# Performance work log

Hardware: AMD Instinct MI355X
Metric: run time of the kernel (lower is better)

## Reference

```python
import jax, jax.numpy as jnp
import numpy as np

D = 768       # GATv2 in/out feats (num_heads=1)
D_OUT = 384   # fc output
K = 51        # round(top_rate * L) = round(0.1 * 512)
EPS = 1e-5    # nn.LayerNorm default eps


def _layer_norm(x, g, b):
    mu = jnp.mean(x, axis=-1, keepdims=True)
    var = jnp.mean((x - mu) ** 2, axis=-1, keepdims=True)
    return (x - mu) / jnp.sqrt(var + EPS) * g + b


def setup_inputs() -> dict:
    key = jax.random.key(0)
    ks = jax.random.split(key, 12)
    B, L = 4, 512
    s = 0.02
    return {
        "hidden_state": jax.random.normal(ks[0], (B, L, D), jnp.float32),
        "attention": jax.random.uniform(ks[1], (B, L, L), jnp.float32),
        # GATv2Conv params (fc_src, fc_dst, attn vector, output bias)
        "W_src": jax.random.normal(ks[2], (D, D), jnp.float32) * s,
        "b_src": jnp.zeros((D,), jnp.float32),
        "W_dst": jax.random.normal(ks[3], (D, D), jnp.float32) * s,
        "b_dst": jnp.zeros((D,), jnp.float32),
        "attn_vec": jax.random.normal(ks[4], (D,), jnp.float32) * s,
        "gat_bias": jnp.zeros((D,), jnp.float32),
        # GlobalAttentionPooling gate_nn: Linear(768, 1)
        "gate_W": jax.random.normal(ks[5], (D, 1), jnp.float32) * s,
        "gate_b": jnp.zeros((1,), jnp.float32),
        # LayerNorm(768)
        "ln_g": jnp.ones((D,), jnp.float32),
        "ln_b": jnp.zeros((D,), jnp.float32),
        # fc: Linear(768, 384)
        "fc_W": jax.random.normal(ks[6], (D, D_OUT), jnp.float32) * s,
        "fc_b": jnp.zeros((D_OUT,), jnp.float32),
        # LayerNorm(384)
        "ln2_g": jnp.ones((D_OUT,), jnp.float32),
        "ln2_b": jnp.zeros((D_OUT,), jnp.float32),
        "mask": jnp.ones((B, L), jnp.int32),  # unused by the original forward
        "type": 0,                              # unused string/type flag
    }


def reference(hidden_state, attention, W_src, b_src, W_dst, b_dst, attn_vec,
              gat_bias, gate_W, gate_b, ln_g, ln_b, fc_W, fc_b, ln2_g, ln2_b,
              mask, type):
    B, L, _ = hidden_state.shape
    # --- topk sparsification: each node i keeps K source neighbors ---
    vals, idx = jax.lax.top_k(attention, K)          # [B, L, K]
    valid = vals > 0.0                                # edges kept by pos_sign filter

    # --- GATv2Conv (num_heads=1, residual=Identity since 768==768) ---
    feat_src = hidden_state @ W_src + b_src           # [B, L, D]
    feat_dst = hidden_state @ W_dst + b_dst           # [B, L, D]
    g = feat_src[jnp.arange(B)[:, None, None], idx]   # [B, L, K, D] gathered src feats
    e = jax.nn.leaky_relu(g + feat_dst[:, :, None, :], 0.2)
    scores = jnp.einsum("blkd,d->blk", e, attn_vec)   # [B, L, K]
    scores = jnp.where(valid, scores, -1e9)           # removed edges masked out
    a = jax.nn.softmax(scores, axis=-1)               # edge_softmax per dst node
    h = jnp.einsum("blk,blkd->bld", a, g)             # weighted scatter-sum
    h = h + hidden_state + gat_bias                   # residual (identity) + bias
    h = jax.nn.leaky_relu(h, 0.01)                    # nn.LeakyReLU activation

    # --- GlobalAttentionPooling: softmax(gate) weighted segment reduce ---
    gate = h @ gate_W + gate_b                        # [B, L, 1]
    p = jax.nn.softmax(gate, axis=1)
    pooled = jnp.sum(p * h, axis=1)                   # [B, D]

    # --- head: fc(dropout(ln(relu(out)))) then ln2 (dropout = eval identity) ---
    out = _layer_norm(jax.nn.relu(pooled), ln_g, ln_b)
    out = out @ fc_W + fc_b
    out = _layer_norm(out, ln2_g, ln2_b)
    return out
```

## Files before the change

### kernel.cpp

```cpp
#include <hip/hip_runtime.h>
#include <math.h>

#define D 768
#define DOUT 384
#define LSEQ 512
#define BATCH 4
#define KTOP 51
#define EPS 1e-5f

typedef unsigned short ushort_t;
typedef __bf16 bf16x8 __attribute__((ext_vector_type(8)));
typedef float f32x4 __attribute__((ext_vector_type(4)));

#define GLOAD16(gp, lp)                                                        \
    __builtin_amdgcn_global_load_lds(                                          \
        (const __attribute__((address_space(1))) unsigned int*)(gp),           \
        (__attribute__((address_space(3))) unsigned int*)(lp), 16, 0, 0)

__device__ __forceinline__ ushort_t f2bf(float f) {
    unsigned int u = __builtin_bit_cast(unsigned int, f);
    u = (u + 0x7FFFu + ((u >> 16) & 1u)) >> 16;
    return (ushort_t)u;
}

__device__ __forceinline__ float bf2f(ushort_t u) {
    unsigned int v = ((unsigned int)u) << 16;
    return __builtin_bit_cast(float, v);
}

__global__ __launch_bounds__(256) void prep_kernel(const float* __restrict__ hidden,
                                                   ushort_t* __restrict__ Ah,
                                                   const float* __restrict__ W0,
                                                   const float* __restrict__ W1,
                                                   ushort_t* __restrict__ WT0,
                                                   ushort_t* __restrict__ WT1,
                                                   float* __restrict__ pooled,
                                                   float* __restrict__ z) {
    __shared__ float tile[32][33];
    const int bid = blockIdx.x;
    const int tid = threadIdx.x;
    if (bid < 1536) {
        const int i = (bid * 256 + tid) * 4;
        const float4 v = *(const float4*)(hidden + i);
        ushort4 o;
        o.x = f2bf(v.x); o.y = f2bf(v.y); o.z = f2bf(v.z); o.w = f2bf(v.w);
        *(ushort4*)(Ah + i) = o;
    } else if (bid < 2688) {
        const int t = bid - 1536;
        const int zz = t / 576;
        const int rem = t - zz * 576;
        const int by = rem / 24, bx = rem - by * 24;
        const float* W = zz ? W1 : W0;
        ushort_t* WT = zz ? WT1 : WT0;
        const int kbase = by * 32;
        const int nbase = bx * 32;
        const int r = tid >> 3, c4 = (tid & 7) * 4;

        const float4 v = *(const float4*)(W + (size_t)(kbase + r) * D + nbase + c4);
        tile[r][c4 + 0] = v.x; tile[r][c4 + 1] = v.y;
        tile[r][c4 + 2] = v.z; tile[r][c4 + 3] = v.w;
        __syncthreads();
        ushort4 o;
        o.x = f2bf(tile[c4 + 0][r]); o.y = f2bf(tile[c4 + 1][r]);
        o.z = f2bf(tile[c4 + 2][r]); o.w = f2bf(tile[c4 + 3][r]);
        *(ushort4*)(WT + (size_t)(nbase + r) * D + kbase + c4) = o;
    } else {
        for (int i = tid; i < BATCH * D; i += 256) pooled[i] = 0.f;
        for (int i = tid; i < BATCH * DOUT; i += 256) z[i] = 0.f;
    }
}

__global__ __launch_bounds__(256) void feat_gemm_kernel(const ushort_t* __restrict__ Ah,
                                                        const ushort_t* __restrict__ WT0,
                                                        const float* __restrict__ b0,
                                                        ushort_t* __restrict__ Csrc_bf,
                                                        const ushort_t* __restrict__ WT1,
                                                        const float* __restrict__ b1,
                                                        float* __restrict__ Cdst) {
    const ushort_t* WT = blockIdx.z ? WT1 : WT0;
    const float* bias = blockIdx.z ? b1 : b0;

    __shared__ ushort_t As[64 * 64];
    __shared__ ushort_t Bs[64 * 64];

    const int tid = threadIdx.x;
    const int lane = tid & 63;
    const int wave = tid >> 6;
    const int quad = lane >> 4;
    const int m15 = lane & 15;
    const int qRow = (wave & 1) * 32;
    const int qCol = (wave >> 1) * 32;

    const int rowBase = blockIdx.y * 64;
    const int colBase = blockIdx.x * 64;

    const int e0 = tid * 8;
    const int r0 = e0 >> 6;
    const int c0 = e0 & 63;
    const int cc = c0 >> 3;
    const int csw = (cc ^ (r0 & 7)) << 3;
    const ushort_t* Abase = Ah + (size_t)rowBase * D;
    const ushort_t* Bbase = WT + (size_t)colBase * D;

    f32x4 acc[2][2] = {};

    for (int kk = 0; kk < D; kk += 64) {
        __syncthreads();
        GLOAD16(Abase + (size_t)r0 * D + kk + csw, &As[e0]);
        GLOAD16(Abase + (size_t)(r0 + 32) * D + kk + csw, &As[e0 + 2048]);
        GLOAD16(Bbase + (size_t)r0 * D + kk + csw, &Bs[e0]);
        GLOAD16(Bbase + (size_t)(r0 + 32) * D + kk + csw, &Bs[e0 + 2048]);
        __syncthreads();

        bf16x8 a[2][2], b[2][2];
#pragma unroll
        for (int i = 0; i < 2; ++i) {
            const int row = qRow + i * 16 + m15;
            const int sw = row & 7;
#pragma unroll
            for (int ks = 0; ks < 2; ++ks)
                a[i][ks] = *(const bf16x8*)&As[row * 64 + ((((ks << 2) + quad) ^ sw) << 3)];
        }
#pragma unroll
        for (int j = 0; j < 2; ++j) {
            const int row = qCol + j * 16 + m15;
            const int sw = row & 7;
#pragma unroll
            for (int ks = 0; ks < 2; ++ks)
                b[j][ks] = *(const bf16x8*)&Bs[row * 64 + ((((ks << 2) + quad) ^ sw) << 3)];
        }
#pragma unroll
        for (int ks = 0; ks < 2; ++ks)
#pragma unroll
            for (int i = 0; i < 2; ++i)
#pragma unroll
                for (int j = 0; j < 2; ++j)
                    acc[i][j] = __builtin_amdgcn_mfma_f32_16x16x32_bf16(a[i][ks], b[j][ks], acc[i][j], 0, 0, 0);
    }

    if (blockIdx.z == 0) {
#pragma unroll
        for (int j = 0; j < 2; ++j) {
            const int col = colBase + qCol + j * 16 + m15;
            const float bv = bias[col];
#pragma unroll
            for (int i = 0; i < 2; ++i) {
                ushort_t* Cp = Csrc_bf + (size_t)(rowBase + qRow + i * 16 + quad * 4) * D + col;
#pragma unroll
                for (int r = 0; r < 4; ++r)
                    Cp[(size_t)r * D] = f2bf(acc[i][j][r] + bv);
            }
        }
    } else {
#pragma unroll
        for (int j = 0; j < 2; ++j) {
            const int col = colBase + qCol + j * 16 + m15;
            const float bv = bias[col];
#pragma unroll
            for (int i = 0; i < 2; ++i) {
                float* Cp = Cdst + (size_t)(rowBase + qRow + i * 16 + quad * 4) * D + col;
#pragma unroll
                for (int r = 0; r < 4; ++r)
                    Cp[(size_t)r * D] = acc[i][j][r] + bv;
            }
        }
    }
}

__global__ __launch_bounds__(256) void score_kernel(const float* __restrict__ attn,
                                                    const ushort_t* __restrict__ fsrc_bf,
                                                    const float* __restrict__ feat_dst,
                                                    const float* __restrict__ attn_vec,
                                                    float* __restrict__ kprob,
                                                    int* __restrict__ kidx) {
    const int row = blockIdx.x;
    const int b = row >> 9;
    const int tid = threadIdx.x;
    const int lane = tid & 63;
    const int wave = tid >> 6;

    __shared__ float vals[LSEQ];
    __shared__ float cval[320];
    __shared__ int   cidx[320];
    __shared__ int   nhi, outSlot;
    __shared__ float sc[KTOP];
    __shared__ int   kid[KTOP];
    __shared__ float kvv[KTOP];

    if (tid == 0) { nhi = 0; outSlot = 0; }

    const float* a = attn + (size_t)row * LSEQ;
    const float v0 = a[tid];
    const float v1 = a[tid + 256];
    vals[tid] = v0;
    vals[tid + 256] = v1;
    __syncthreads();

    if (v0 > 0.75f) {
        const int s = atomicAdd(&nhi, 1);
        if (s < 320) { cval[s] = v0; cidx[s] = tid; }
    }
    if (v1 > 0.75f) {
        const int s = atomicAdd(&nhi, 1);
        if (s < 320) { cval[s] = v1; cidx[s] = tid + 256; }
    }
    __syncthreads();

    const int n = nhi;
    if (n >= KTOP && n <= 320) {
        if (tid < n) {
            const float v = cval[tid];
            const int e = cidx[tid];
            int r = 0;
            for (int j = 0; j < n; ++j) {
                const float u = cval[j];
                r += (u > v) || (u == v && cidx[j] < e);
            }
            if (r < KTOP) {
                const int s = atomicAdd(&outSlot, 1);
                kid[s] = e; kvv[s] = v;
            }
        }
    } else {
#pragma unroll
        for (int e0 = 0; e0 < 2; ++e0) {
            const int e = tid + e0 * 256;
            const float v = vals[e];
            int r = 0;
            for (int j = 0; j < LSEQ; ++j) {
                const float u = vals[j];
                r += (u > v) || (u == v && j < e);
            }
            if (r < KTOP) {
                const int s = atomicAdd(&outSlot, 1);
                kid[s] = e; kvv[s] = v;
            }
        }
    }

    const float* fdp = feat_dst + (size_t)row * D;
    float fdr[16], avr[16];
    {
        const int d0 = lane * 8;
        const float4 f0 = *(const float4*)(fdp + d0);
        const float4 f1 = *(const float4*)(fdp + d0 + 4);
        const float4 a0 = *(const float4*)(attn_vec + d0);
        const float4 a1 = *(const float4*)(attn_vec + d0 + 4);
        fdr[0]=f0.x; fdr[1]=f0.y; fdr[2]=f0.z; fdr[3]=f0.w;
        fdr[4]=f1.x; fdr[5]=f1.y; fdr[6]=f1.z; fdr[7]=f1.w;
        avr[0]=a0.x; avr[1]=a0.y; avr[2]=a0.z; avr[3]=a0.w;
        avr[4]=a1.x; avr[5]=a1.y; avr[6]=a1.z; avr[7]=a1.w;
    }
    if (lane < 32) {
        const int d1 = (lane + 64) * 8;
        const float4 f0 = *(const float4*)(fdp + d1);
        const float4 f1 = *(const float4*)(fdp + d1 + 4);
        const float4 a0 = *(const float4*)(attn_vec + d1);
        const float4 a1 = *(const float4*)(attn_vec + d1 + 4);
        fdr[8]=f0.x; fdr[9]=f0.y; fdr[10]=f0.z; fdr[11]=f0.w;
        fdr[12]=f1.x; fdr[13]=f1.y; fdr[14]=f1.z; fdr[15]=f1.w;
        avr[8]=a0.x; avr[9]=a0.y; avr[10]=a0.z; avr[11]=a0.w;
        avr[12]=a1.x; avr[13]=a1.y; avr[14]=a1.z; avr[15]=a1.w;
    }
    __syncthreads();

    for (int k = wave; k < KTOP; k += 4) {
        const ushort_t* g = fsrc_bf + ((size_t)(b << 9) + kid[k]) * D;
        float s = 0.f;
        const bf16x8 g0 = *(const bf16x8*)(g + lane * 8);
#pragma unroll
        for (int jj = 0; jj < 8; ++jj) {
            float x = (float)g0[jj] + fdr[jj];
            x = x > 0.f ? x : 0.2f * x;
            s += x * avr[jj];
        }
        if (lane < 32) {
            const bf16x8 g1 = *(const bf16x8*)(g + (lane + 64) * 8);
#pragma unroll
            for (int jj = 0; jj < 8; ++jj) {
                float x = (float)g1[jj] + fdr[8 + jj];
                x = x > 0.f ? x : 0.2f * x;
                s += x * avr[8 + jj];
            }
        }
#pragma unroll
        for (int off = 32; off > 0; off >>= 1) s += __shfl_down(s, off);
        if (lane == 0) sc[k] = (kvv[k] > 0.f) ? s : -1e9f;
    }
    __syncthreads();

    if (wave == 0) {
        float s = (lane < KTOP) ? sc[lane] : -3.0e38f;
        float m = s;
#pragma unroll
        for (int off = 32; off > 0; off >>= 1) m = fmaxf(m, __shfl_xor(m, off));
        float e = (lane < KTOP) ? __expf(s - m) : 0.f;
        float sum = e;
#pragma unroll
        for (int off = 32; off > 0; off >>= 1) sum += __shfl_xor(sum, off);
        if (lane < KTOP) sc[lane] = e / sum;
    }
    __syncthreads();

    if (tid < KTOP) {
        kprob[(size_t)row * 64 + tid] = sc[tid];
        kidx[(size_t)row * 64 + tid]  = kid[tid];
    }
}

__global__ __launch_bounds__(256) void gath_kernel(const float* __restrict__ kprob,
                                                   const int* __restrict__ kidx,
                                                   const ushort_t* __restrict__ fsrc,
                                                   const float* __restrict__ gat_bias,
                                                   const float* __restrict__ hidden,
                                                   const float* __restrict__ gate_W,
                                                   const float* __restrict__ gate_b,
                                                   ushort_t* __restrict__ h,
                                                   float* __restrict__ gate) {
    const int w = threadIdx.x >> 6;
    const int lane = threadIdx.x & 63;
    const int row = blockIdx.x * 4 + w;
    const int b = row >> 9;

    __shared__ float ps[4][KTOP];
    __shared__ int   is_[4][KTOP];
    if (lane < KTOP) {
        ps[w][lane]  = kprob[(size_t)row * 64 + lane];
        is_[w][lane] = kidx[(size_t)row * 64 + lane];
    }
    __syncthreads();

    const int d0 = lane * 8;
    const int d1 = 512 + lane * 4;
    const ushort_t* fb = fsrc + ((size_t)(b << 9)) * D;

    float acc[12] = {};
    for (int k = 0; k < KTOP; ++k) {
        const float p = ps[w][k];
        const ushort_t* g = fb + (size_t)is_[w][k] * D;
        const bf16x8 g0 = *(const bf16x8*)(g + d0);
        const ushort4 g1 = *(const ushort4*)(g + d1);
#pragma unroll
        for (int jj = 0; jj < 8; ++jj) acc[jj] += p * (float)g0[jj];
        acc[8]  += p * bf2f(g1.x);
        acc[9]  += p * bf2f(g1.y);
        acc[10] += p * bf2f(g1.z);
        acc[11] += p * bf2f(g1.w);
    }

    const float* hid = hidden + (size_t)row * D;
    const float4 h0 = *(const float4*)(hid + d0);
    const float4 h1 = *(const float4*)(hid + d0 + 4);
    const float4 h2 = *(const float4*)(hid + d1);
    const float4 b0 = *(const float4*)(gat_bias + d0);
    const float4 b1 = *(const float4*)(gat_bias + d0 + 4);
    const float4 b2 = *(const float4*)(gat_bias + d1);
    const float4 w0 = *(const float4*)(gate_W + d0);
    const float4 w1 = *(const float4*)(gate_W + d0 + 4);
    const float4 w2 = *(const float4*)(gate_W + d1);

    float v[12], gw[12];
    v[0]=acc[0]+h0.x+b0.x; v[1]=acc[1]+h0.y+b0.y; v[2]=acc[2]+h0.z+b0.z; v[3]=acc[3]+h0.w+b0.w;
    v[4]=acc[4]+h1.x+b1.x; v[5]=acc[5]+h1.y+b1.y; v[6]=acc[6]+h1.z+b1.z; v[7]=acc[7]+h1.w+b1.w;
    v[8]=acc[8]+h2.x+b2.x; v[9]=acc[9]+h2.y+b2.y; v[10]=acc[10]+h2.z+b2.z; v[11]=acc[11]+h2.w+b2.w;
    gw[0]=w0.x; gw[1]=w0.y; gw[2]=w0.z; gw[3]=w0.w;
    gw[4]=w1.x; gw[5]=w1.y; gw[6]=w1.z; gw[7]=w1.w;
    gw[8]=w2.x; gw[9]=w2.y; gw[10]=w2.z; gw[11]=w2.w;

    float dot = 0.f;
#pragma unroll
    for (int jj = 0; jj < 12; ++jj) {
        float x = v[jj];
        x = x > 0.f ? x : 0.01f * x;
        v[jj] = x;
        dot += x * gw[jj];
    }

    ushort_t* hb = h + (size_t)row * D;
    ushort4 o;
    o.x = f2bf(v[0]); o.y = f2bf(v[1]); o.z = f2bf(v[2]); o.w = f2bf(v[3]);
    *(ushort4*)(hb + d0) = o;
    o.x = f2bf(v[4]); o.y = f2bf(v[5]); o.z = f2bf(v[6]); o.w = f2bf(v[7]);
    *(ushort4*)(hb + d0 + 4) = o;
    o.x = f2bf(v[8]); o.y = f2bf(v[9]); o.z = f2bf(v[10]); o.w = f2bf(v[11]);
    *(ushort4*)(hb + d1) = o;

#pragma unroll
    for (int off = 32; off > 0; off >>= 1) dot += __shfl_down(dot, off);
    if (lane == 0) gate[row] = gate_b[0] + dot;
}

__global__ __launch_bounds__(256) void pool_kernel(const ushort_t* __restrict__ h,
                                                   const float* __restrict__ gate,
                                                   float* __restrict__ pooled) {
    const int b = blockIdx.z;
    const int lbase = blockIdx.y * 64;
    const int d = blockIdx.x * 256 + threadIdx.x;
    const int tid = threadIdx.x;
    const int lane = tid & 63;
    const int w = tid >> 6;

    __shared__ float wred[4];
    __shared__ float ps[64];

    const float g0 = gate[b * LSEQ + tid];
    const float g1 = gate[b * LSEQ + tid + 256];
    float m = fmaxf(g0, g1);
#pragma unroll
    for (int off = 32; off > 0; off >>= 1) m = fmaxf(m, __shfl_xor(m, off));
    if (lane == 0) wred[w] = m;
    __syncthreads();
    m = fmaxf(fmaxf(wred[0], wred[1]), fmaxf(wred[2], wred[3]));
    float e = __expf(g0 - m) + __expf(g1 - m);
#pragma unroll
    for (int off = 32; off > 0; off >>= 1) e += __shfl_xor(e, off);
    __syncthreads();
    if (lane == 0) wred[w] = e;
    __syncthreads();
    const float inv = 1.f / (wred[0] + wred[1] + wred[2] + wred[3]);
    if (tid < 64) ps[tid] = __expf(gate[b * LSEQ + lbase + tid] - m) * inv;
    __syncthreads();

    const ushort_t* hb = h + ((size_t)(b * LSEQ + lbase)) * D + d;
    float acc = 0.f;
#pragma unroll 8
    for (int l = 0; l < 64; ++l) {
        acc += ps[l] * bf2f(hb[(size_t)l * D]);
    }
    atomicAdd(&pooled[b * D + d], acc);
}

__global__ __launch_bounds__(256) void fc_kernel(const float* __restrict__ pooled,
                                                 const float* __restrict__ ln_g,
                                                 const float* __restrict__ ln_b,
                                                 const float* __restrict__ fc_W,
                                                 float* __restrict__ z) {
    const int b = blockIdx.z;
    const int by = blockIdx.y;
    const int dbase = by * 256;
    const int jbase = blockIdx.x * 64;
    const int tid = threadIdx.x;
    const int lane = tid & 63;
    const int w = tid >> 6;
    const int jt = tid & 63;
    const int sub = tid >> 6;

    __shared__ float wred[4];
    __shared__ float ys[256];
    __shared__ float part[4][64];

    float v[3];
#pragma unroll
    for (int i = 0; i < 3; ++i) v[i] = fmaxf(pooled[b * D + tid + i * 256], 0.f);

    float s = v[0] + v[1] + v[2];
#pragma unroll
    for (int off = 32; off > 0; off >>= 1) s += __shfl_xor(s, off);
    if (lane == 0) wred[w] = s;
    __syncthreads();
    const float mu = (wred[0] + wred[1] + wred[2] + wred[3]) / (float)D;
    float vs = 0.f;
#pragma unroll
    for (int i = 0; i < 3; ++i) { const float dd = v[i] - mu; vs += dd * dd; }
#pragma unroll
    for (int off = 32; off > 0; off >>= 1) vs += __shfl_xor(vs, off);
    __syncthreads();
    if (lane == 0) wred[w] = vs;
    __syncthreads();
    const float rstd = rsqrtf((wred[0] + wred[1] + wred[2] + wred[3]) / (float)D + EPS);

    const float vb = (by == 0) ? v[0] : (by == 1 ? v[1] : v[2]);
    ys[tid] = (vb - mu) * rstd * ln_g[dbase + tid] + ln_b[dbase + tid];
    __syncthreads();

    const float* W = fc_W + (size_t)(dbase + sub * 64) * DOUT + jbase + jt;
    const float* yy = ys + sub * 64;
    float acc = 0.f;
#pragma unroll 8
    for (int i = 0; i < 64; ++i) {
        acc += yy[i] * W[(size_t)i * DOUT];
    }
    part[sub][jt] = acc;
    __syncthreads();
    if (sub == 0) {
        const float tot = part[0][jt] + part[1][jt] + part[2][jt] + part[3][jt];
        atomicAdd(&z[b * DOUT + jbase + jt], tot);
    }
}

__global__ __launch_bounds__(384) void ln2_kernel(const float* __restrict__ z,
                                                  const float* __restrict__ fc_b,
                                                  const float* __restrict__ ln2_g,
                                                  const float* __restrict__ ln2_b,
                                                  float* __restrict__ out) {
    const int b = blockIdx.x;
    const int tid = threadIdx.x;
    const int lane = tid & 63;
    const int wave = tid >> 6;
    __shared__ float wred[6];

    const float v = z[b * DOUT + tid] + fc_b[tid];

    float s = v;
#pragma unroll
    for (int off = 32; off > 0; off >>= 1) s += __shfl_xor(s, off);
    if (lane == 0) wred[wave] = s;
    __syncthreads();
    float mu = 0.f;
#pragma unroll
    for (int w = 0; w < 6; ++w) mu += wred[w];
    mu /= (float)DOUT;
    __syncthreads();

    const float dd = v - mu;
    float s2 = dd * dd;
#pragma unroll
    for (int off = 32; off > 0; off >>= 1) s2 += __shfl_xor(s2, off);
    if (lane == 0) wred[wave] = s2;
    __syncthreads();
    float var = 0.f;
#pragma unroll
    for (int w = 0; w < 6; ++w) var += wred[w];
    const float rstd = rsqrtf(var / (float)DOUT + EPS);

    out[b * DOUT + tid] = dd * rstd * ln2_g[tid] + ln2_b[tid];
}

extern "C" void kernel_launch(void* const* d_in, const int* in_sizes, int n_in,
                              void* d_out, int out_size, void* d_ws, size_t ws_size,
                              hipStream_t stream) {
    const float* hidden   = (const float*)d_in[0];
    const float* attention= (const float*)d_in[1];
    const float* W_src    = (const float*)d_in[2];
    const float* b_src    = (const float*)d_in[3];
    const float* W_dst    = (const float*)d_in[4];
    const float* b_dst    = (const float*)d_in[5];
    const float* attn_vec = (const float*)d_in[6];
    const float* gat_bias = (const float*)d_in[7];
    const float* gate_W   = (const float*)d_in[8];
    const float* gate_b   = (const float*)d_in[9];
    const float* ln_g     = (const float*)d_in[10];
    const float* ln_b     = (const float*)d_in[11];
    const float* fc_W     = (const float*)d_in[12];
    const float* fc_b     = (const float*)d_in[13];
    const float* ln2_g    = (const float*)d_in[14];
    const float* ln2_b    = (const float*)d_in[15];
    float* out = (float*)d_out;

    const int M = BATCH * LSEQ;
    float* feat_dst = (float*)d_ws;
    float* gate     = feat_dst + (size_t)M * D;
    float* pooled   = gate + M;
    float* z        = pooled + BATCH * D;
    float* kprob    = z + BATCH * DOUT;
    int*   kidx     = (int*)(kprob + (size_t)M * 64);
    ushort_t* Ah    = (ushort_t*)(kidx + (size_t)M * 64);
    ushort_t* WT0   = Ah + (size_t)M * D;
    ushort_t* WT1   = WT0 + (size_t)D * D;
    ushort_t* fsrcb = WT1 + (size_t)D * D;
    ushort_t* h     = fsrcb + (size_t)M * D;

    hipLaunchKernelGGL(prep_kernel, dim3(2689), dim3(256), 0, stream,
                       hidden, Ah, W_src, W_dst, WT0, WT1, pooled, z);
    hipLaunchKernelGGL(feat_gemm_kernel, dim3(D / 64, M / 64, 2), dim3(256), 0, stream,
                       Ah, WT0, b_src, fsrcb, WT1, b_dst, feat_dst);
    hipLaunchKernelGGL(score_kernel, dim3(M), dim3(256), 0, stream,
                       attention, fsrcb, feat_dst, attn_vec, kprob, kidx);
    hipLaunchKernelGGL(gath_kernel, dim3(M / 4), dim3(256), 0, stream,
                       kprob, kidx, fsrcb, gat_bias, hidden, gate_W, gate_b, h, gate);
    hipLaunchKernelGGL(pool_kernel, dim3(D / 256, LSEQ / 64, BATCH), dim3(256), 0, stream,
                       h, gate, pooled);
    hipLaunchKernelGGL(fc_kernel, dim3(DOUT / 64, D / 256, BATCH), dim3(256), 0, stream,
                       pooled, ln_g, ln_b, fc_W, z);
    hipLaunchKernelGGL(ln2_kernel, dim3(BATCH), dim3(384), 0, stream,
                       z, fc_b, ln2_g, ln2_b, out);
}
```

Before: 172.4 us.

## Fuse score and gather with online softmax; merge tail into cooperative kernel

Merges the edge-score and weighted-gather kernels into one, using an online per-wave softmax so each gathered source row is read once and the kprob/kidx buffers disappear. It also replaces the pool, fc and ln2 launches with one cooperative kernel of 96 blocks that uses grid-wide syncs between stages. The aim is to cut repeated gather traffic and launch overhead. In exchange it adds 12 KB of shared memory per block in the fused kernel and relies on the cost of cooperative grid syncs.

Result: slower. 208.1 us (+20.7%).

```diff
diff --git a/kernel.cpp b/kernel.cpp
--- a/kernel.cpp
+++ b/kernel.cpp
@@ -1,5 +1,8 @@
 #include <hip/hip_runtime.h>
+#include <hip/hip_cooperative_groups.h>
 #include <math.h>
+
+namespace cg = cooperative_groups;
 
 #define D 768
 #define DOUT 384
@@ -167,12 +170,16 @@
     }
 }
 
-__global__ __launch_bounds__(256) void score_kernel(const float* __restrict__ attn,
-                                                    const ushort_t* __restrict__ fsrc_bf,
-                                                    const float* __restrict__ feat_dst,
-                                                    const float* __restrict__ attn_vec,
-                                                    float* __restrict__ kprob,
-                                                    int* __restrict__ kidx) {
+__global__ __launch_bounds__(256) void scoregath_kernel(const float* __restrict__ attn,
+                                                        const ushort_t* __restrict__ fsrc_bf,
+                                                        const float* __restrict__ feat_dst,
+                                                        const float* __restrict__ attn_vec,
+                                                        const float* __restrict__ gat_bias,
+                                                        const float* __restrict__ hidden,
+                                                        const float* __restrict__ gate_W,
+                                                        const float* __restrict__ gate_b,
+                                                        ushort_t* __restrict__ h,
+                                                        float* __restrict__ gate) {
     const int row = blockIdx.x;
     const int b = row >> 9;
     const int tid = threadIdx.x;
@@ -183,9 +190,11 @@
     __shared__ float cval[320];
     __shared__ int   cidx[320];
     __shared__ int   nhi, outSlot;
-    __shared__ float sc[KTOP];
     __shared__ int   kid[KTOP];
     __shared__ float kvv[KTOP];
+    __shared__ float wm[4], wl[4];
+    __shared__ float hpart[4][D];
+    __shared__ float gred[4];
 
     if (tid == 0) { nhi = 0; outSlot = 0; }
 
@@ -264,266 +273,217 @@
     }
     __syncthreads();
 
+    float m_run = -3.0e38f, l_run = 0.f;
+    float acc[16] = {};
     for (int k = wave; k < KTOP; k += 4) {
         const ushort_t* g = fsrc_bf + ((size_t)(b << 9) + kid[k]) * D;
+        const bf16x8 g0 = *(const bf16x8*)(g + lane * 8);
+        bf16x8 g1 = {};
+        if (lane < 32) g1 = *(const bf16x8*)(g + (lane + 64) * 8);
+
+        float gf[16];
         float s = 0.f;
-        const bf16x8 g0 = *(const bf16x8*)(g + lane * 8);
 #pragma unroll
         for (int jj = 0; jj < 8; ++jj) {
-            float x = (float)g0[jj] + fdr[jj];
+            gf[jj] = (float)g0[jj];
+            float x = gf[jj] + fdr[jj];
             x = x > 0.f ? x : 0.2f * x;
             s += x * avr[jj];
         }
+#pragma unroll
+        for (int jj = 0; jj < 8; ++jj) gf[8 + jj] = (float)g1[jj];
         if (lane < 32) {
-            const bf16x8 g1 = *(const bf16x8*)(g + (lane + 64) * 8);
 #pragma unroll
             for (int jj = 0; jj < 8; ++jj) {
-                float x = (float)g1[jj] + fdr[8 + jj];
+                float x = gf[8 + jj] + fdr[8 + jj];
                 x = x > 0.f ? x : 0.2f * x;
                 s += x * avr[8 + jj];
             }
         }
 #pragma unroll
-        for (int off = 32; off > 0; off >>= 1) s += __shfl_down(s, off);
-        if (lane == 0) sc[k] = (kvv[k] > 0.f) ? s : -1e9f;
+        for (int off = 32; off > 0; off >>= 1) s += __shfl_xor(s, off);
+        s = (kvv[k] > 0.f) ? s : -1e9f;
+
+        const float mn = fmaxf(m_run, s);
+        const float rs = __expf(m_run - mn);
+        const float p = __expf(s - mn);
+        l_run = l_run * rs + p;
+#pragma unroll
+        for (int jj = 0; jj < 16; ++jj) acc[jj] = acc[jj] * rs + p * gf[jj];
+        m_run = mn;
+    }
+
+    if (lane == 0) { wm[wave] = m_run; wl[wave] = l_run; }
+#pragma unroll
+    for (int jj = 0; jj < 8; ++jj) hpart[wave][lane * 8 + jj] = acc[jj];
+    if (lane < 32) {
+#pragma unroll
+        for (int jj = 0; jj < 8; ++jj) hpart[wave][(lane + 64) * 8 + jj] = acc[8 + jj];
     }
     __syncthreads();
 
-    if (wave == 0) {
-        float s = (lane < KTOP) ? sc[lane] : -3.0e38f;
-        float m = s;
-#pragma unroll
-        for (int off = 32; off > 0; off >>= 1) m = fmaxf(m, __shfl_xor(m, off));
-        float e = (lane < KTOP) ? __expf(s - m) : 0.f;
-        float sum = e;
-#pragma unroll
-        for (int off = 32; off > 0; off >>= 1) sum += __shfl_xor(sum, off);
-        if (lane < KTOP) sc[lane] = e / sum;
-    }
+    const float M = fmaxf(fmaxf(wm[0], wm[1]), fmaxf(wm[2], wm[3]));
+    const float r0 = __expf(wm[0] - M), r1 = __expf(wm[1] - M);
+    const float r2 = __expf(wm[2] - M), r3 = __expf(wm[3] - M);
+    const float invL = 1.f / (r0 * wl[0] + r1 * wl[1] + r2 * wl[2] + r3 * wl[3]);
+
+    float dotp = 0.f;
+    const float* hid = hidden + (size_t)row * D;
+    ushort_t* hb = h + (size_t)row * D;
+#pragma unroll
+    for (int j = 0; j < 3; ++j) {
+        const int d = tid + j * 256;
+        const float hv = (r0 * hpart[0][d] + r1 * hpart[1][d] +
+                          r2 * hpart[2][d] + r3 * hpart[3][d]) * invL;
+        float v = hv + hid[d] + gat_bias[d];
+        v = v > 0.f ? v : 0.01f * v;
+        hb[d] = f2bf(v);
+        dotp += v * gate_W[d];
+    }
+#pragma unroll
+    for (int off = 32; off > 0; off >>= 1) dotp += __shfl_xor(dotp, off);
+    if (lane == 0) gred[wave] = dotp;
     __syncthreads();
-
-    if (tid < KTOP) {
-        kprob[(size_t)row * 64 + tid] = sc[tid];
-        kidx[(size_t)row * 64 + tid]  = kid[tid];
-    }
-}
-
-__global__ __launch_bounds__(256) void gath_kernel(const float* __restrict__ kprob,
-                                                   const int* __restrict__ kidx,
-                                                   const ushort_t* __restrict__ fsrc,
-                                                   const float* __restrict__ gat_bias,
-                                                   const float* __restrict__ hidden,
-                                                   const float* __restrict__ gate_W,
-                                                   const float* __restrict__ gate_b,
-                                                   ushort_t* __restrict__ h,
-                                                   float* __restrict__ gate) {
-    const int w = threadIdx.x >> 6;
-    const int lane = threadIdx.x & 63;
-    const int row = blockIdx.x * 4 + w;
-    const int b = row >> 9;
-
-    __shared__ float ps[4][KTOP];
-    __shared__ int   is_[4][KTOP];
-    if (lane < KTOP) {
-        ps[w][lane]  = kprob[(size_t)row * 64 + lane];
-        is_[w][lane] = kidx[(size_t)row * 64 + lane];
-    }
-    __syncthreads();
-
-    const int d0 = lane * 8;
-    const int d1 = 512 + lane * 4;
-    const ushort_t* fb = fsrc + ((size_t)(b << 9)) * D;
-
-    float acc[12] = {};
-    for (int k = 0; k < KTOP; ++k) {
-        const float p = ps[w][k];
-        const ushort_t* g = fb + (size_t)is_[w][k] * D;
-        const bf16x8 g0 = *(const bf16x8*)(g + d0);
-        const ushort4 g1 = *(const ushort4*)(g + d1);
-#pragma unroll
-        for (int jj = 0; jj < 8; ++jj) acc[jj] += p * (float)g0[jj];
-        acc[8]  += p * bf2f(g1.x);
-        acc[9]  += p * bf2f(g1.y);
-        acc[10] += p * bf2f(g1.z);
-        acc[11] += p * bf2f(g1.w);
-    }
-
-    const float* hid = hidden + (size_t)row * D;
-    const float4 h0 = *(const float4*)(hid + d0);
-    const float4 h1 = *(const float4*)(hid + d0 + 4);
-    const float4 h2 = *(const float4*)(hid + d1);
-    const float4 b0 = *(const float4*)(gat_bias + d0);
-    const float4 b1 = *(const float4*)(gat_bias + d0 + 4);
-    const float4 b2 = *(const float4*)(gat_bias + d1);
-    const float4 w0 = *(const float4*)(gate_W + d0);
-    const float4 w1 = *(const float4*)(gate_W + d0 + 4);
-    const float4 w2 = *(const float4*)(gate_W + d1);
-
-    float v[12], gw[12];
-    v[0]=acc[0]+h0.x+b0.x; v[1]=acc[1]+h0.y+b0.y; v[2]=acc[2]+h0.z+b0.z; v[3]=acc[3]+h0.w+b0.w;
-    v[4]=acc[4]+h1.x+b1.x; v[5]=acc[5]+h1.y+b1.y; v[6]=acc[6]+h1.z+b1.z; v[7]=acc[7]+h1.w+b1.w;
-    v[8]=acc[8]+h2.x+b2.x; v[9]=acc[9]+h2.y+b2.y; v[10]=acc[10]+h2.z+b2.z; v[11]=acc[11]+h2.w+b2.w;
-    gw[0]=w0.x; gw[1]=w0.y; gw[2]=w0.z; gw[3]=w0.w;
-    gw[4]=w1.x; gw[5]=w1.y; gw[6]=w1.z; gw[7]=w1.w;
-    gw[8]=w2.x; gw[9]=w2.y; gw[10]=w2.z; gw[11]=w2.w;
-
-    float dot = 0.f;
-#pragma unroll
-    for (int jj = 0; jj < 12; ++jj) {
-        float x = v[jj];
-        x = x > 0.f ? x : 0.01f * x;
-        v[jj] = x;
-        dot += x * gw[jj];
-    }
-
-    ushort_t* hb = h + (size_t)row * D;
-    ushort4 o;
-    o.x = f2bf(v[0]); o.y = f2bf(v[1]); o.z = f2bf(v[2]); o.w = f2bf(v[3]);
-    *(ushort4*)(hb + d0) = o;
-    o.x = f2bf(v[4]); o.y = f2bf(v[5]); o.z = f2bf(v[6]); o.w = f2bf(v[7]);
-    *(ushort4*)(hb + d0 + 4) = o;
-    o.x = f2bf(v[8]); o.y = f2bf(v[9]); o.z = f2bf(v[10]); o.w = f2bf(v[11]);
-    *(ushort4*)(hb + d1) = o;
-
-#pragma unroll
-    for (int off = 32; off > 0; off >>= 1) dot += __shfl_down(dot, off);
-    if (lane == 0) gate[row] = gate_b[0] + dot;
-}
-
-__global__ __launch_bounds__(256) void pool_kernel(const ushort_t* __restrict__ h,
+    if (tid == 0) gate[row] = gate_b[0] + gred[0] + gred[1] + gred[2] + gred[3];
+}
+
+__global__ __launch_bounds__(256) void tail_kernel(const ushort_t* __restrict__ h,
                                                    const float* __restrict__ gate,
-                                                   float* __restrict__ pooled) {
-    const int b = blockIdx.z;
-    const int lbase = blockIdx.y * 64;
-    const int d = blockIdx.x * 256 + threadIdx.x;
+                                                   float* __restrict__ pooled,
+                                                   const float* __restrict__ ln_g,
+                                                   const float* __restrict__ ln_b,
+                                                   const float* __restrict__ fc_W,
+                                                   float* __restrict__ z,
+                                                   const float* __restrict__ fc_b,
+                                                   const float* __restrict__ ln2_g,
+                                                   const float* __restrict__ ln2_b,
+                                                   float* __restrict__ out) {
+    cg::grid_group grid = cg::this_grid();
+    const int bid = blockIdx.x;
     const int tid = threadIdx.x;
     const int lane = tid & 63;
     const int w = tid >> 6;
 
     __shared__ float wred[4];
     __shared__ float ps[64];
-
-    const float g0 = gate[b * LSEQ + tid];
-    const float g1 = gate[b * LSEQ + tid + 256];
-    float m = fmaxf(g0, g1);
-#pragma unroll
-    for (int off = 32; off > 0; off >>= 1) m = fmaxf(m, __shfl_xor(m, off));
-    if (lane == 0) wred[w] = m;
-    __syncthreads();
-    m = fmaxf(fmaxf(wred[0], wred[1]), fmaxf(wred[2], wred[3]));
-    float e = __expf(g0 - m) + __expf(g1 - m);
-#pragma unroll
-    for (int off = 32; off > 0; off >>= 1) e += __shfl_xor(e, off);
-    __syncthreads();
-    if (lane == 0) wred[w] = e;
-    __syncthreads();
-    const float inv = 1.f / (wred[0] + wred[1] + wred[2] + wred[3]);
-    if (tid < 64) ps[tid] = __expf(gate[b * LSEQ + lbase + tid] - m) * inv;
-    __syncthreads();
-
-    const ushort_t* hb = h + ((size_t)(b * LSEQ + lbase)) * D + d;
-    float acc = 0.f;
-#pragma unroll 8
-    for (int l = 0; l < 64; ++l) {
-        acc += ps[l] * bf2f(hb[(size_t)l * D]);
-    }
-    atomicAdd(&pooled[b * D + d], acc);
-}
-
-__global__ __launch_bounds__(256) void fc_kernel(const float* __restrict__ pooled,
-                                                 const float* __restrict__ ln_g,
-                                                 const float* __restrict__ ln_b,
-                                                 const float* __restrict__ fc_W,
-                                                 float* __restrict__ z) {
-    const int b = blockIdx.z;
-    const int by = blockIdx.y;
-    const int dbase = by * 256;
-    const int jbase = blockIdx.x * 64;
-    const int tid = threadIdx.x;
-    const int lane = tid & 63;
-    const int w = tid >> 6;
-    const int jt = tid & 63;
-    const int sub = tid >> 6;
-
-    __shared__ float wred[4];
     __shared__ float ys[256];
     __shared__ float part[4][64];
 
-    float v[3];
-#pragma unroll
-    for (int i = 0; i < 3; ++i) v[i] = fmaxf(pooled[b * D + tid + i * 256], 0.f);
-
-    float s = v[0] + v[1] + v[2];
-#pragma unroll
-    for (int off = 32; off > 0; off >>= 1) s += __shfl_xor(s, off);
-    if (lane == 0) wred[w] = s;
-    __syncthreads();
-    const float mu = (wred[0] + wred[1] + wred[2] + wred[3]) / (float)D;
-    float vs = 0.f;
-#pragma unroll
-    for (int i = 0; i < 3; ++i) { const float dd = v[i] - mu; vs += dd * dd; }
-#pragma unroll
-    for (int off = 32; off > 0; off >>= 1) vs += __shfl_xor(vs, off);
-    __syncthreads();
-    if (lane == 0) wred[w] = vs;
-    __syncthreads();
-    const float rstd = rsqrtf((wred[0] + wred[1] + wred[2] + wred[3]) / (float)D + EPS);
-
-    const float vb = (by == 0) ? v[0] : (by == 1 ? v[1] : v[2]);
-    ys[tid] = (vb - mu) * rstd * ln_g[dbase + tid] + ln_b[dbase + tid];
-    __syncthreads();
-
-    const float* W = fc_W + (size_t)(dbase + sub * 64) * DOUT + jbase + jt;
-    const float* yy = ys + sub * 64;
-    float acc = 0.f;
+    {
+        const int dc = bid % 3;
+        const int lc = (bid / 3) & 7;
+        const int b = bid / 24;
+        const int lbase = lc * 64;
+        const int d = dc * 256 + tid;
+
+        const float g0 = gate[b * LSEQ + tid];
+        const float g1 = gate[b * LSEQ + tid + 256];
+        float m = fmaxf(g0, g1);
+#pragma unroll
+        for (int off = 32; off > 0; off >>= 1) m = fmaxf(m, __shfl_xor(m, off));
+        if (lane == 0) wred[w] = m;
+        __syncthreads();
+        m = fmaxf(fmaxf(wred[0], wred[1]), fmaxf(wred[2], wred[3]));
+        float e = __expf(g0 - m) + __expf(g1 - m);
+#pragma unroll
+        for (int off = 32; off > 0; off >>= 1) e += __shfl_xor(e, off);
+        __syncthreads();
+        if (lane == 0) wred[w] = e;
+        __syncthreads();
+        const float inv = 1.f / (wred[0] + wred[1] + wred[2] + wred[3]);
+        if (tid < 64) ps[tid] = __expf(gate[b * LSEQ + lbase + tid] - m) * inv;
+        __syncthreads();
+
+        const ushort_t* hb = h + ((size_t)(b * LSEQ + lbase)) * D + d;
+        float acc = 0.f;
 #pragma unroll 8
-    for (int i = 0; i < 64; ++i) {
-        acc += yy[i] * W[(size_t)i * DOUT];
-    }
-    part[sub][jt] = acc;
-    __syncthreads();
-    if (sub == 0) {
-        const float tot = part[0][jt] + part[1][jt] + part[2][jt] + part[3][jt];
-        atomicAdd(&z[b * DOUT + jbase + jt], tot);
-    }
-}
-
-__global__ __launch_bounds__(384) void ln2_kernel(const float* __restrict__ z,
-                                                  const float* __restrict__ fc_b,
-                                                  const float* __restrict__ ln2_g,
-                                                  const float* __restrict__ ln2_b,
-                                                  float* __restrict__ out) {
-    const int b = blockIdx.x;
-    const int tid = threadIdx.x;
-    const int lane = tid & 63;
-    const int wave = tid >> 6;
-    __shared__ float wred[6];
-
-    const float v = z[b * DOUT + tid] + fc_b[tid];
-
-    float s = v;
-#pragma unroll
-    for (int off = 32; off > 0; off >>= 1) s += __shfl_xor(s, off);
-    if (lane == 0) wred[wave] = s;
-    __syncthreads();
-    float mu = 0.f;
-#pragma unroll
-    for (int w = 0; w < 6; ++w) mu += wred[w];
-    mu /= (float)DOUT;
-    __syncthreads();
-
-    const float dd = v - mu;
-    float s2 = dd * dd;
-#pragma unroll
-    for (int off = 32; off > 0; off >>= 1) s2 += __shfl_xor(s2, off);
-    if (lane == 0) wred[wave] = s2;
-    __syncthreads();
-    float var = 0.f;
-#pragma unroll
-    for (int w = 0; w < 6; ++w) var += wred[w];
-    const float rstd = rsqrtf(var / (float)DOUT + EPS);
-
-    out[b * DOUT + tid] = dd * rstd * ln2_g[tid] + ln2_b[tid];
+        for (int l = 0; l < 64; ++l) {
+            acc += ps[l] * bf2f(hb[(size_t)l * D]);
+        }
+        atomicAdd(&pooled[b * D + d], acc);
+    }
+
+    grid.sync();
+
+    if (bid < 72) {
+        const int jx = bid % 6;
+        const int by = (bid / 6) % 3;
+        const int b = bid / 18;
+        const int dbase = by * 256;
+        const int jbase = jx * 64;
+        const int jt = tid & 63;
+        const int sub = tid >> 6;
+
+        float v[3];
+#pragma unroll
+        for (int i = 0; i < 3; ++i) v[i] = fmaxf(pooled[b * D + tid + i * 256], 0.f);
+
+        float s = v[0] + v[1] + v[2];
+#pragma unroll
+        for (int off = 32; off > 0; off >>= 1) s += __shfl_xor(s, off);
+        __syncthreads();
+        if (lane == 0) wred[w] = s;
+        __syncthreads();
+        const float mu = (wred[0] + wred[1] + wred[2] + wred[3]) / (float)D;
+        float vs = 0.f;
+#pragma unroll
+        for (int i = 0; i < 3; ++i) { const float dd = v[i] - mu; vs += dd * dd; }
+#pragma unroll
+        for (int off = 32; off > 0; off >>= 1) vs += __shfl_xor(vs, off);
+        __syncthreads();
+        if (lane == 0) wred[w] = vs;
+        __syncthreads();
+        const float rstd = rsqrtf((wred[0] + wred[1] + wred[2] + wred[3]) / (float)D + EPS);
+
+        const float vb = (by == 0) ? v[0] : (by == 1 ? v[1] : v[2]);
+        ys[tid] = (vb - mu) * rstd * ln_g[dbase + tid] + ln_b[dbase + tid];
+        __syncthreads();
+
+        const float* W = fc_W + (size_t)(dbase + sub * 64) * DOUT + jbase + jt;
+        const float* yy = ys + sub * 64;
+        float acc = 0.f;
+#pragma unroll 8
+        for (int i = 0; i < 64; ++i) {
+            acc += yy[i] * W[(size_t)i * DOUT];
+        }
+        part[sub][jt] = acc;
+        __syncthreads();
+        if (sub == 0) {
+            const float tot = part[0][jt] + part[1][jt] + part[2][jt] + part[3][jt];
+            atomicAdd(&z[b * DOUT + jbase + jt], tot);
+        }
+    }
+
+    grid.sync();
+
+    if (bid < 4) {
+        const int b = bid;
+        const bool has2 = tid < (DOUT - 256);
+        const float v0 = z[b * DOUT + tid] + fc_b[tid];
+        const float v1 = has2 ? z[b * DOUT + tid + 256] + fc_b[tid + 256] : 0.f;
+
+        float s = v0 + v1;
+#pragma unroll
+        for (int off = 32; off > 0; off >>= 1) s += __shfl_xor(s, off);
+        __syncthreads();
+        if (lane == 0) wred[w] = s;
+        __syncthreads();
+        const float mu = (wred[0] + wred[1] + wred[2] + wred[3]) / (float)DOUT;
+
+        const float d0 = v0 - mu;
+        const float d1 = v1 - mu;
+        float s2 = d0 * d0 + (has2 ? d1 * d1 : 0.f);
+#pragma unroll
+        for (int off = 32; off > 0; off >>= 1) s2 += __shfl_xor(s2, off);
+        __syncthreads();
+        if (lane == 0) wred[w] = s2;
+        __syncthreads();
+        const float rstd = rsqrtf((wred[0] + wred[1] + wred[2] + wred[3]) / (float)DOUT + EPS);
+
+        out[b * DOUT + tid] = d0 * rstd * ln2_g[tid] + ln2_b[tid];
+        if (has2)
+            out[b * DOUT + tid + 256] = d1 * rstd * ln2_g[tid + 256] + ln2_b[tid + 256];
+    }
 }
 
 extern "C" void kernel_launch(void* const* d_in, const int* in_sizes, int n_in,
@@ -552,9 +512,7 @@
     float* gate     = feat_dst + (size_t)M * D;
     float* pooled   = gate + M;
     float* z        = pooled + BATCH * D;
-    float* kprob    = z + BATCH * DOUT;
-    int*   kidx     = (int*)(kprob + (size_t)M * 64);
-    ushort_t* Ah    = (ushort_t*)(kidx + (size_t)M * 64);
+    ushort_t* Ah    = (ushort_t*)(z + BATCH * DOUT);
     ushort_t* WT0   = Ah + (size_t)M * D;
     ushort_t* WT1   = WT0 + (size_t)D * D;
     ushort_t* fsrcb = WT1 + (size_t)D * D;
@@ -564,14 +522,13 @@
                        hidden, Ah, W_src, W_dst, WT0, WT1, pooled, z);
     hipLaunchKernelGGL(feat_gemm_kernel, dim3(D / 64, M / 64, 2), dim3(256), 0, stream,
                        Ah, WT0, b_src, fsrcb, WT1, b_dst, feat_dst);
-    hipLaunchKernelGGL(score_kernel, dim3(M), dim3(256), 0, stream,
-                       attention, fsrcb, feat_dst, attn_vec, kprob, kidx);
-    hipLaunchKernelGGL(gath_kernel, dim3(M / 4), dim3(256), 0, stream,
-                       kprob, kidx, fsrcb, gat_bias, hidden, gate_W, gate_b, h, gate);
-    hipLaunchKernelGGL(pool_kernel, dim3(D / 256, LSEQ / 64, BATCH), dim3(256), 0, stream,
-                       h, gate, pooled);
-    hipLaunchKernelGGL(fc_kernel, dim3(DOUT / 64, D / 256, BATCH), dim3(256), 0, stream,
-                       pooled, ln_g, ln_b, fc_W, z);
-    hipLaunchKernelGGL(ln2_kernel, dim3(BATCH), dim3(384), 0, stream,
-                       z, fc_b, ln2_g, ln2_b, out);
-}
+    hipLaunchKernelGGL(scoregath_kernel, dim3(M), dim3(256), 0, stream,
+                       attention, fsrcb, feat_dst, attn_vec, gat_bias, hidden,
+                       gate_W, gate_b, h, gate);
+
+    void* tail_args[] = {(void*)&h, (void*)&gate, (void*)&pooled,
+                         (void*)&ln_g, (void*)&ln_b, (void*)&fc_W, (void*)&z,
+                         (void*)&fc_b, (void*)&ln2_g, (void*)&ln2_b, (void*)&out};
+    hipLaunchCooperativeKernel((void*)tail_kernel, dim3(96), dim3(256),
+                               tail_args, 0, stream);
+}
```

## Fuse score and gather kernels, splitting neighbor aggregation across waves via LDS atomics

Applied to the files above, without the earlier changes.

Merges the per-row score/top-k kernel and the weighted gather kernel into one block per destination row. The kprob/kidx round trip through global memory and one launch go away. The gather work is split across the four waves, and partial sums are combined with shared-memory atomics into a padded LDS buffer that reuses the top-k scratch space. It also reworks the score lane layout so every lane handles 12 features with no divergent half-wave branch. The cost is extra LDS atomics and barriers per row, and the second pass over gathered source rows now runs inside the same block.

After: 191.2 us. 10.9% more time.

```diff
diff --git a/kernel.cpp b/kernel.cpp
--- a/kernel.cpp
+++ b/kernel.cpp
@@ -27,6 +27,8 @@
     unsigned int v = ((unsigned int)u) << 16;
     return __builtin_bit_cast(float, v);
 }
+
+__device__ __forceinline__ int hpad(int d) { return d + (d >> 5); }
 
 __global__ __launch_bounds__(256) void prep_kernel(const float* __restrict__ hidden,
                                                    ushort_t* __restrict__ Ah,
@@ -167,25 +169,33 @@
     }
 }
 
-__global__ __launch_bounds__(256) void score_kernel(const float* __restrict__ attn,
-                                                    const ushort_t* __restrict__ fsrc_bf,
-                                                    const float* __restrict__ feat_dst,
-                                                    const float* __restrict__ attn_vec,
-                                                    float* __restrict__ kprob,
-                                                    int* __restrict__ kidx) {
+__global__ __launch_bounds__(256) void scoregath_kernel(const float* __restrict__ attn,
+                                                        const ushort_t* __restrict__ fsrc_bf,
+                                                        const float* __restrict__ feat_dst,
+                                                        const float* __restrict__ attn_vec,
+                                                        const float* __restrict__ gat_bias,
+                                                        const float* __restrict__ hidden,
+                                                        const float* __restrict__ gate_W,
+                                                        const float* __restrict__ gate_b,
+                                                        ushort_t* __restrict__ h,
+                                                        float* __restrict__ gate) {
     const int row = blockIdx.x;
     const int b = row >> 9;
     const int tid = threadIdx.x;
     const int lane = tid & 63;
     const int wave = tid >> 6;
 
-    __shared__ float vals[LSEQ];
-    __shared__ float cval[320];
+    __shared__ float bufA[832];
     __shared__ int   cidx[320];
     __shared__ int   nhi, outSlot;
-    __shared__ float sc[KTOP];
     __shared__ int   kid[KTOP];
     __shared__ float kvv[KTOP];
+    __shared__ float sc[KTOP];
+    __shared__ float gred[4];
+
+    float* vals = bufA;
+    float* cval = bufA + 512;
+    float* harr = bufA;
 
     if (tid == 0) { nhi = 0; outSlot = 0; }
 
@@ -238,53 +248,47 @@
         }
     }
 
+    const int d0 = lane * 8;
+    const int d1 = 512 + lane * 4;
     const float* fdp = feat_dst + (size_t)row * D;
-    float fdr[16], avr[16];
+    float fdr[12], avr[12];
     {
-        const int d0 = lane * 8;
         const float4 f0 = *(const float4*)(fdp + d0);
         const float4 f1 = *(const float4*)(fdp + d0 + 4);
+        const float4 f2 = *(const float4*)(fdp + d1);
         const float4 a0 = *(const float4*)(attn_vec + d0);
         const float4 a1 = *(const float4*)(attn_vec + d0 + 4);
-        fdr[0]=f0.x; fdr[1]=f0.y; fdr[2]=f0.z; fdr[3]=f0.w;
-        fdr[4]=f1.x; fdr[5]=f1.y; fdr[6]=f1.z; fdr[7]=f1.w;
-        avr[0]=a0.x; avr[1]=a0.y; avr[2]=a0.z; avr[3]=a0.w;
-        avr[4]=a1.x; avr[5]=a1.y; avr[6]=a1.z; avr[7]=a1.w;
-    }
-    if (lane < 32) {
-        const int d1 = (lane + 64) * 8;
-        const float4 f0 = *(const float4*)(fdp + d1);
-        const float4 f1 = *(const float4*)(fdp + d1 + 4);
-        const float4 a0 = *(const float4*)(attn_vec + d1);
-        const float4 a1 = *(const float4*)(attn_vec + d1 + 4);
-        fdr[8]=f0.x; fdr[9]=f0.y; fdr[10]=f0.z; fdr[11]=f0.w;
-        fdr[12]=f1.x; fdr[13]=f1.y; fdr[14]=f1.z; fdr[15]=f1.w;
-        avr[8]=a0.x; avr[9]=a0.y; avr[10]=a0.z; avr[11]=a0.w;
-        avr[12]=a1.x; avr[13]=a1.y; avr[14]=a1.z; avr[15]=a1.w;
-    }
-    __syncthreads();
-
+        const float4 a2 = *(const float4*)(attn_vec + d1);
+        fdr[0]=f0.x; fdr[1]=f0.y; fdr[2]=f0.z;  fdr[3]=f0.w;
+        fdr[4]=f1.x; fdr[5]=f1.y; fdr[6]=f1.z;  fdr[7]=f1.w;
+        fdr[8]=f2.x; fdr[9]=f2.y; fdr[10]=f2.z; fdr[11]=f2.w;
+        avr[0]=a0.x; avr[1]=a0.y; avr[2]=a0.z;  avr[3]=a0.w;
+        avr[4]=a1.x; avr[5]=a1.y; avr[6]=a1.z;  avr[7]=a1.w;
+        avr[8]=a2.x; avr[9]=a2.y; avr[10]=a2.z; avr[11]=a2.w;
+    }
+    __syncthreads();
+
+    const ushort_t* fb = fsrc_bf + ((size_t)(b << 9)) * D;
     for (int k = wave; k < KTOP; k += 4) {
-        const ushort_t* g = fsrc_bf + ((size_t)(b << 9) + kid[k]) * D;
+        const ushort_t* g = fb + (size_t)kid[k] * D;
+        const bf16x8 g0 = *(const bf16x8*)(g + d0);
+        const ushort4 g1 = *(const ushort4*)(g + d1);
         float s = 0.f;
-        const bf16x8 g0 = *(const bf16x8*)(g + lane * 8);
 #pragma unroll
         for (int jj = 0; jj < 8; ++jj) {
             float x = (float)g0[jj] + fdr[jj];
             x = x > 0.f ? x : 0.2f * x;
             s += x * avr[jj];
         }
-        if (lane < 32) {
-            const bf16x8 g1 = *(const bf16x8*)(g + (lane + 64) * 8);
-#pragma unroll
-            for (int jj = 0; jj < 8; ++jj) {
-                float x = (float)g1[jj] + fdr[8 + jj];
-                x = x > 0.f ? x : 0.2f * x;
-                s += x * avr[8 + jj];
-            }
-        }
-#pragma unroll
-        for (int off = 32; off > 0; off >>= 1) s += __shfl_down(s, off);
+        {
+            float x;
+            x = bf2f(g1.x) + fdr[8];  x = x > 0.f ? x : 0.2f * x; s += x * avr[8];
+            x = bf2f(g1.y) + fdr[9];  x = x > 0.f ? x : 0.2f * x; s += x * avr[9];
+            x = bf2f(g1.z) + fdr[10]; x = x > 0.f ? x : 0.2f * x; s += x * avr[10];
+            x = bf2f(g1.w) + fdr[11]; x = x > 0.f ? x : 0.2f * x; s += x * avr[11];
+        }
+#pragma unroll
+        for (int off = 32; off > 0; off >>= 1) s += __shfl_xor(s, off);
         if (lane == 0) sc[k] = (kvv[k] > 0.f) ? s : -1e9f;
     }
     __syncthreads();
@@ -299,45 +303,15 @@
 #pragma unroll
         for (int off = 32; off > 0; off >>= 1) sum += __shfl_xor(sum, off);
         if (lane < KTOP) sc[lane] = e / sum;
-    }
-    __syncthreads();
-
-    if (tid < KTOP) {
-        kprob[(size_t)row * 64 + tid] = sc[tid];
-        kidx[(size_t)row * 64 + tid]  = kid[tid];
-    }
-}
-
-__global__ __launch_bounds__(256) void gath_kernel(const float* __restrict__ kprob,
-                                                   const int* __restrict__ kidx,
-                                                   const ushort_t* __restrict__ fsrc,
-                                                   const float* __restrict__ gat_bias,
-                                                   const float* __restrict__ hidden,
-                                                   const float* __restrict__ gate_W,
-                                                   const float* __restrict__ gate_b,
-                                                   ushort_t* __restrict__ h,
-                                                   float* __restrict__ gate) {
-    const int w = threadIdx.x >> 6;
-    const int lane = threadIdx.x & 63;
-    const int row = blockIdx.x * 4 + w;
-    const int b = row >> 9;
-
-    __shared__ float ps[4][KTOP];
-    __shared__ int   is_[4][KTOP];
-    if (lane < KTOP) {
-        ps[w][lane]  = kprob[(size_t)row * 64 + lane];
-        is_[w][lane] = kidx[(size_t)row * 64 + lane];
-    }
-    __syncthreads();
-
-    const int d0 = lane * 8;
-    const int d1 = 512 + lane * 4;
-    const ushort_t* fb = fsrc + ((size_t)(b << 9)) * D;
+    } else {
+        for (int i = tid - 64; i < 791; i += 192) harr[i] = 0.f;
+    }
+    __syncthreads();
 
     float acc[12] = {};
-    for (int k = 0; k < KTOP; ++k) {
-        const float p = ps[w][k];
-        const ushort_t* g = fb + (size_t)is_[w][k] * D;
+    for (int k = wave; k < KTOP; k += 4) {
+        const float p = sc[k];
+        const ushort_t* g = fb + (size_t)kid[k] * D;
         const bf16x8 g0 = *(const bf16x8*)(g + d0);
         const ushort4 g1 = *(const ushort4*)(g + d1);
 #pragma unroll
@@ -347,47 +321,28 @@
         acc[10] += p * bf2f(g1.z);
         acc[11] += p * bf2f(g1.w);
     }
-
+#pragma unroll
+    for (int jj = 0; jj < 8; ++jj) atomicAdd(&harr[hpad(d0 + jj)], acc[jj]);
+#pragma unroll
+    for (int jj = 0; jj < 4; ++jj) atomicAdd(&harr[hpad(d1 + jj)], acc[8 + jj]);
+    __syncthreads();
+
+    float dotp = 0.f;
     const float* hid = hidden + (size_t)row * D;
-    const float4 h0 = *(const float4*)(hid + d0);
-    const float4 h1 = *(const float4*)(hid + d0 + 4);
-    const float4 h2 = *(const float4*)(hid + d1);
-    const float4 b0 = *(const float4*)(gat_bias + d0);
-    const float4 b1 = *(const float4*)(gat_bias + d0 + 4);
-    const float4 b2 = *(const float4*)(gat_bias + d1);
-    const float4 w0 = *(const float4*)(gate_W + d0);
-    const float4 w1 = *(const float4*)(gate_W + d0 + 4);
-    const float4 w2 = *(const float4*)(gate_W + d1);
-
-    float v[12], gw[12];
-    v[0]=acc[0]+h0.x+b0.x; v[1]=acc[1]+h0.y+b0.y; v[2]=acc[2]+h0.z+b0.z; v[3]=acc[3]+h0.w+b0.w;
-    v[4]=acc[4]+h1.x+b1.x; v[5]=acc[5]+h1.y+b1.y; v[6]=acc[6]+h1.z+b1.z; v[7]=acc[7]+h1.w+b1.w;
-    v[8]=acc[8]+h2.x+b2.x; v[9]=acc[9]+h2.y+b2.y; v[10]=acc[10]+h2.z+b2.z; v[11]=acc[11]+h2.w+b2.w;
-    gw[0]=w0.x; gw[1]=w0.y; gw[2]=w0.z; gw[3]=w0.w;
-    gw[4]=w1.x; gw[5]=w1.y; gw[6]=w1.z; gw[7]=w1.w;
-    gw[8]=w2.x; gw[9]=w2.y; gw[10]=w2.z; gw[11]=w2.w;
-
-    float dot = 0.f;
-#pragma unroll
-    for (int jj = 0; jj < 12; ++jj) {
-        float x = v[jj];
-        x = x > 0.f ? x : 0.01f * x;
-        v[jj] = x;
-        dot += x * gw[jj];
-    }
-
     ushort_t* hb = h + (size_t)row * D;
-    ushort4 o;
-    o.x = f2bf(v[0]); o.y = f2bf(v[1]); o.z = f2bf(v[2]); o.w = f2bf(v[3]);
-    *(ushort4*)(hb + d0) = o;
-    o.x = f2bf(v[4]); o.y = f2bf(v[5]); o.z = f2bf(v[6]); o.w = f2bf(v[7]);
-    *(ushort4*)(hb + d0 + 4) = o;
-    o.x = f2bf(v[8]); o.y = f2bf(v[9]); o.z = f2bf(v[10]); o.w = f2bf(v[11]);
-    *(ushort4*)(hb + d1) = o;
-
-#pragma unroll
-    for (int off = 32; off > 0; off >>= 1) dot += __shfl_down(dot, off);
-    if (lane == 0) gate[row] = gate_b[0] + dot;
+#pragma unroll
+    for (int j = 0; j < 3; ++j) {
+        const int d = tid + j * 256;
+        float v = harr[hpad(d)] + hid[d] + gat_bias[d];
+        v = v > 0.f ? v : 0.01f * v;
+        hb[d] = f2bf(v);
+        dotp += v * gate_W[d];
+    }
+#pragma unroll
+    for (int off = 32; off > 0; off >>= 1) dotp += __shfl_xor(dotp, off);
+    if (lane == 0) gred[wave] = dotp;
+    __syncthreads();
+    if (tid == 0) gate[row] = gate_b[0] + gred[0] + gred[1] + gred[2] + gred[3];
 }
 
 __global__ __launch_bounds__(256) void pool_kernel(const ushort_t* __restrict__ h,
@@ -552,9 +507,7 @@
     float* gate     = feat_dst + (size_t)M * D;
     float* pooled   = gate + M;
     float* z        = pooled + BATCH * D;
-    float* kprob    = z + BATCH * DOUT;
-    int*   kidx     = (int*)(kprob + (size_t)M * 64);
-    ushort_t* Ah    = (ushort_t*)(kidx + (size_t)M * 64);
+    ushort_t* Ah    = (ushort_t*)(z + BATCH * DOUT);
     ushort_t* WT0   = Ah + (size_t)M * D;
     ushort_t* WT1   = WT0 + (size_t)D * D;
     ushort_t* fsrcb = WT1 + (size_t)D * D;
@@ -564,10 +517,9 @@
                        hidden, Ah, W_src, W_dst, WT0, WT1, pooled, z);
     hipLaunchKernelGGL(feat_gemm_kernel, dim3(D / 64, M / 64, 2), dim3(256), 0, stream,
                        Ah, WT0, b_src, fsrcb, WT1, b_dst, feat_dst);
-    hipLaunchKernelGGL(score_kernel, dim3(M), dim3(256), 0, stream,
-                       attention, fsrcb, feat_dst, attn_vec, kprob, kidx);
-    hipLaunchKernelGGL(gath_kernel, dim3(M / 4), dim3(256), 0, stream,
-                       kprob, kidx, fsrcb, gat_bias, hidden, gate_W, gate_b, h, gate);
+    hipLaunchKernelGGL(scoregath_kernel, dim3(M), dim3(256), 0, stream,
+                       attention, fsrcb, feat_dst, attn_vec, gat_bias, hidden,
+                       gate_W, gate_b, h, gate);
     hipLaunchKernelGGL(pool_kernel, dim3(D / 256, LSEQ / 64, BATCH), dim3(256), 0, stream,
                        h, gate, pooled);
     hipLaunchKernelGGL(fc_kernel, dim3(DOUT / 64, D / 256, BATCH), dim3(256), 0, stream,
```
